# Kernel tuning notes

Hardware: AMD Instinct MI355X
Metric: run time of the kernel (lower is better)

Reference implementation:

```python
import jax, jax.numpy as jnp
import numpy as np

N_NODES = 50000
N_EDGES = 800000
EMB = 128
N_LAYERS = 2
BN_EPS = 1e-5


def setup_inputs() -> dict:
    key = jax.random.key(0)
    ks = jax.random.split(key, 16)
    N, E, D, L = N_NODES, N_EDGES, EMB, N_LAYERS
    x = jax.random.randint(ks[0], (N, 2), 0, 3)
    edge_index = jax.random.randint(ks[1], (2, E), 0, N)
    edge_attr = jax.random.randint(ks[2], (E, 2), 0, 3)
    batch = jnp.zeros((N,), dtype=jnp.int32)
    s = 0.1
    xemb1 = jax.random.normal(ks[3], (120, D)) * s   # atom-type embedding
    xemb2 = jax.random.normal(ks[4], (3, D)) * s     # chirality embedding
    e1 = jax.random.normal(ks[5], (L, 7, D)) * s     # bond-type embedding per layer
    e2 = jax.random.normal(ks[6], (L, 3, D)) * s     # bond-direction embedding per layer
    W1 = jax.random.normal(ks[7], (L, D, 2 * D)) * s
    b1 = jnp.zeros((L, 2 * D))
    W2 = jax.random.normal(ks[8], (L, 2 * D, D)) * s
    b2 = jnp.zeros((L, D))
    gamma = jnp.ones((L, D))
    beta = jnp.zeros((L, D))
    return {"x": x, "edge_index": edge_index, "edge_attr": edge_attr, "batch": batch,
            "xemb1": xemb1, "xemb2": xemb2, "e1": e1, "e2": e2,
            "W1": W1, "b1": b1, "W2": W2, "b2": b2, "gamma": gamma, "beta": beta}


def _gnn_forward(x, edge_index, edge_attr, xemb1, xemb2, e1, e2, W1, b1, W2, b2, gamma, beta):
    N = x.shape[0]
    # add self loops; self-loop edge_attr = [4, 0]
    loop = jnp.arange(N, dtype=edge_index.dtype)
    src = jnp.concatenate([edge_index[0], loop])
    dst = jnp.concatenate([edge_index[1], loop])
    loop_attr = jnp.concatenate([jnp.full((N, 1), 4, dtype=edge_attr.dtype),
                                 jnp.zeros((N, 1), dtype=edge_attr.dtype)], axis=1)
    ea = jnp.concatenate([edge_attr, loop_attr], axis=0)  # [E+N, 2]

    # input node embedding
    h = xemb1[x[:, 0]] + xemb2[x[:, 1]]  # [N, D]

    for l in range(N_LAYERS):
        eemb = e1[l][ea[:, 0]] + e2[l][ea[:, 1]]      # [E+N, D]
        msg = h[src] + eemb                            # gather + edge fuse
        agg = jax.ops.segment_sum(msg, dst, num_segments=N)  # scatter-add
        # GIN update MLP: Linear -> ReLU -> Linear
        h2 = jax.nn.relu(agg @ W1[l] + b1[l]) @ W2[l] + b2[l]
        # BatchNorm1d (training mode: biased batch stats)
        mu = jnp.mean(h2, axis=0)
        var = jnp.mean(jnp.square(h2 - mu), axis=0)
        h2 = gamma[l] * (h2 - mu) * jax.lax.rsqrt(var + BN_EPS) + beta[l]
        # dropout(relu) for non-final layers; drop_ratio=0 -> identity dropout
        h = h2 if l == N_LAYERS - 1 else jax.nn.relu(h2)
    return h  # JK='last'


def reference(x, edge_index, edge_attr, batch, xemb1, xemb2, e1, e2, W1, b1, W2, b2, gamma, beta):
    return _gnn_forward(x, edge_index, edge_attr, xemb1, xemb2, e1, e2, W1, b1, W2, b2, gamma, beta)
```

## Files before the change

### kernel.cpp

```cpp
#include <hip/hip_runtime.h>
#include <stdint.h>

#define N_NODES 50000
#define N_EDGES 800000
#define EMB 128
#define NPAD 50176
#define MBLK 392
#define BN_EPS 1e-5f
#define SENT_KEY ((N_NODES << 5) | 21)
#define NODES_PER_XCD 6250
#define XCHUNK 2048
#define NCHUNKS ((N_EDGES + XCHUNK - 1) / XCHUNK)

typedef __attribute__((ext_vector_type(8))) short short8;
typedef __attribute__((ext_vector_type(4))) float f32x4;

__device__ __forceinline__ float bf2f(unsigned short u) {
    return __uint_as_float(((unsigned int)u) << 16);
}
__device__ __forceinline__ unsigned short f2bf(float f) {
    unsigned int u = __float_as_uint(f);
    u += 0x7fffu + ((u >> 16) & 1u);
    return (unsigned short)(u >> 16);
}
__device__ __forceinline__ float bflo(unsigned int v) { return __uint_as_float(v << 16); }
__device__ __forceinline__ float bfhi(unsigned int v) { return __uint_as_float(v & 0xffff0000u); }
__device__ __forceinline__ unsigned int packbf(float lo, float hi) {
    return (unsigned int)f2bf(lo) | ((unsigned int)f2bf(hi) << 16);
}

__global__ void k_prep(const int* __restrict__ x, const float* __restrict__ xe1,
                       const float* __restrict__ xe2, unsigned int* __restrict__ h,
                       const float* __restrict__ W1, const float* __restrict__ W2,
                       unsigned short* __restrict__ w1t, unsigned short* __restrict__ w2t,
                       int* __restrict__ deg,
                       const int* __restrict__ ei, const int* __restrict__ ea,
                       int* __restrict__ keyv, float* __restrict__ bnsum) {
    int idx = blockIdx.x * 256 + threadIdx.x;
    int i = idx >> 6, j = idx & 63;
    if (i < N_NODES) {
        int a = x[2 * i], c = x[2 * i + 1];
        float2 va = *(const float2*)(xe1 + a * EMB + j * 2);
        float2 vb = *(const float2*)(xe2 + c * EMB + j * 2);
        h[i * 64 + j] = packbf(va.x + vb.x, va.y + vb.y);
    } else if (i == N_NODES) {
        h[(size_t)i * 64 + j] = 0u;
    }
    if (idx < 4 * 32768) {
        int sec = idx >> 15, q = idx & 32767;
        if (sec < 2) {
            int r = q >> 8, c = q & 255;
            w1t[sec * 32768 + c * 128 + r] = f2bf(W1[sec * 32768 + q]);
        } else {
            int s = sec - 2;
            int r = q >> 7, c = q & 127;
            w2t[s * 32768 + c * 256 + r] = f2bf(W2[s * 32768 + q]);
        }
    }
    if (idx < N_EDGES) {
        int2 aa = *(const int2*)(ea + 2 * idx);
        keyv[idx] = (ei[idx] << 5) | (aa.x * 3 + aa.y);
    }
    if (idx < N_NODES) deg[idx] = 0;
    if (idx < 256) bnsum[idx] = 0.f;
}

__global__ void k_hist(const int* __restrict__ dst, int* __restrict__ deg) {
    int xcd = blockIdx.x & 7, chunk = blockIdx.x >> 3;
    int lo = xcd * NODES_PER_XCD, hi = lo + NODES_PER_XCD;
    int e0 = chunk * XCHUNK + threadIdx.x * 4;
#pragma unroll
    for (int it = 0; it < XCHUNK / 1024; ++it) {
        int e = e0 + it * 1024;
        if (e < N_EDGES) {
            int4 d4 = *(const int4*)(dst + e);
            if (d4.x >= lo && d4.x < hi) atomicAdd(&deg[d4.x], 1);
            if (d4.y >= lo && d4.y < hi) atomicAdd(&deg[d4.y], 1);
            if (d4.z >= lo && d4.z < hi) atomicAdd(&deg[d4.z], 1);
            if (d4.w >= lo && d4.w < hi) atomicAdd(&deg[d4.w], 1);
        }
    }
}

__global__ void k_scan1(const int* __restrict__ deg, int* __restrict__ part, int* __restrict__ bsums) {
    __shared__ int wsum[16];
    int lane = threadIdx.x & 63, wid = threadIdx.x >> 6;
    int i = blockIdx.x * 1024 + threadIdx.x;
    int d = (i < N_NODES) ? deg[i] : 0;
    int v = (d + 15) & ~15;
    int s = v;
#pragma unroll
    for (int off = 1; off < 64; off <<= 1) {
        int t = __shfl_up(s, off);
        if (lane >= off) s += t;
    }
    if (lane == 63) wsum[wid] = s;
    __syncthreads();
    if (wid == 0) {
        int w = (lane < 16) ? wsum[lane] : 0;
#pragma unroll
        for (int off = 1; off < 16; off <<= 1) {
            int t = __shfl_up(w, off);
            if (lane >= off) w += t;
        }
        if (lane < 16) wsum[lane] = w;
    }
    __syncthreads();
    int base = (wid > 0) ? wsum[wid - 1] : 0;
    if (i < N_NODES) part[i] = base + s - v;
    if (threadIdx.x == 1023) bsums[blockIdx.x] = wsum[15];
}

__global__ void k_scan3(const int* __restrict__ part, const int* __restrict__ bsums,
                        const int* __restrict__ deg, int* __restrict__ offs,
                        int* __restrict__ cursor, int* __restrict__ keys) {
    __shared__ int bs[64];
    int tid = threadIdx.x;
    if (tid < 64) {
        int v = (tid < 49) ? bsums[tid] : 0;
        int orig = v;
#pragma unroll
        for (int off = 1; off < 64; off <<= 1) {
            int t = __shfl_up(v, off);
            if (tid >= off) v += t;
        }
        bs[tid] = v - orig;
    }
    __syncthreads();
    int i = blockIdx.x * 256 + tid;
    if (i >= N_NODES) return;
    int o = part[i] + bs[i >> 10];
    offs[i] = o;
    cursor[i] = o;
    int d = deg[i], pd = (d + 15) & ~15;
    for (int j = d; j < pd; ++j) keys[o + j] = SENT_KEY;
    if (i == N_NODES - 1) offs[N_NODES] = o + pd;
}

__global__ void k_fill(const int* __restrict__ dst, const int* __restrict__ keyv,
                       int* __restrict__ cursor, int* __restrict__ keys) {
    int xcd = blockIdx.x & 7, chunk = blockIdx.x >> 3;
    int lo = xcd * NODES_PER_XCD, hi = lo + NODES_PER_XCD;
    int e0 = chunk * XCHUNK + threadIdx.x * 4;
#pragma unroll
    for (int it = 0; it < XCHUNK / 1024; ++it) {
        int e = e0 + it * 1024;
        if (e < N_EDGES) {
            int4 d4 = *(const int4*)(dst + e);
            int dv[4] = {d4.x, d4.y, d4.z, d4.w};
#pragma unroll
            for (int q = 0; q < 4; ++q) {
                int d = dv[q];
                if (d >= lo && d < hi) {
                    int p = atomicAdd(&cursor[d], 1);
                    keys[p] = keyv[e + q];
                }
            }
        }
    }
}

__global__ __launch_bounds__(256) void k_agg(
    const unsigned int* __restrict__ h,
    const int* __restrict__ offs,
    const int* __restrict__ keys,
    const float* __restrict__ e1l, const float* __restrict__ e2l,
    unsigned int* __restrict__ agg)
{
    __shared__ float e12[22 * 132];
    for (int t = threadIdx.x; t < 22 * 128; t += 256) {
        int combo = t >> 7, f = t & 127;
        float v = 0.f;
        if (combo < 21) {
            int a0 = combo / 3, a1 = combo - a0 * 3;
            v = e1l[a0 * EMB + f] + e2l[a1 * EMB + f];
        }
        e12[combo * 132 + f] = v;
    }
    __syncthreads();
    int wave = threadIdx.x >> 6, lane = threadIdx.x & 63;
    int sub = lane >> 4, fl = lane & 15;
    int node = blockIdx.x * 16 + wave * 4 + sub;
    float ax[8] = {0.f, 0.f, 0.f, 0.f, 0.f, 0.f, 0.f, 0.f};
    int o = 0, nch = 0;
    if (node < N_NODES) {
        o = offs[node];
        nch = (offs[node + 1] - o) >> 4;
        uint4 hv = *(const uint4*)(h + (size_t)node * 64 + fl * 4);
        const float* ep = e12 + 12 * 132 + fl * 8;
        float4 e0 = *(const float4*)ep, e1_ = *(const float4*)(ep + 4);
        ax[0] = bflo(hv.x) + e0.x;  ax[1] = bfhi(hv.x) + e0.y;
        ax[2] = bflo(hv.y) + e0.z;  ax[3] = bfhi(hv.y) + e0.w;
        ax[4] = bflo(hv.z) + e1_.x; ax[5] = bfhi(hv.z) + e1_.y;
        ax[6] = bflo(hv.w) + e1_.z; ax[7] = bfhi(hv.w) + e1_.w;
    }
    int maxch = nch;
#pragma unroll
    for (int d = 32; d; d >>= 1) maxch = max(maxch, __shfl_xor(maxch, d));
    int key = (0 < nch) ? keys[o + fl] : SENT_KEY;
    for (int c = 0; c < maxch; ++c) {
        int keyn = (c + 1 < nch) ? keys[o + (c + 1) * 16 + fl] : SENT_KEY;
#pragma unroll
        for (int j = 0; j < 16; ++j) {
            int kj = __shfl(key, sub * 16 + j);
            uint4 g = *(const uint4*)(h + (size_t)(kj >> 5) * 64 + fl * 4);
            const float* ep = e12 + (kj & 31) * 132 + fl * 8;
            float4 e0 = *(const float4*)ep, e1_ = *(const float4*)(ep + 4);
            ax[0] += bflo(g.x) + e0.x;  ax[1] += bfhi(g.x) + e0.y;
            ax[2] += bflo(g.y) + e0.z;  ax[3] += bfhi(g.y) + e0.w;
            ax[4] += bflo(g.z) + e1_.x; ax[5] += bfhi(g.z) + e1_.y;
            ax[6] += bflo(g.w) + e1_.z; ax[7] += bfhi(g.w) + e1_.w;
        }
        key = keyn;
    }
    if (node < NPAD) {
        uint4 out;
        out.x = packbf(ax[0], ax[1]); out.y = packbf(ax[2], ax[3]);
        out.z = packbf(ax[4], ax[5]); out.w = packbf(ax[6], ax[7]);
        *(uint4*)(agg + (size_t)node * 64 + fl * 4) = out;
    }
}

__global__ __launch_bounds__(256, 2) void k_mlp(
    unsigned short* aggh2,
    const unsigned short* __restrict__ w1t,
    const float* __restrict__ b1,
    const unsigned short* __restrict__ w2t,
    const float* __restrict__ b2,
    float* __restrict__ bnsum)
{
    __shared__ float bn[256];
    int lane = threadIdx.x & 63;
    int wave = threadIdx.x >> 6;
    int quad = lane >> 4, r16 = lane & 15;
    int m0 = (blockIdx.x * 4 + wave) * 32;
    int sel  = (lane >> 5) & 1;
    int srcA = ((lane >> 4) & 1) * 32 + r16;
    int srcB = srcA + 16;
    bn[threadIdx.x] = 0.f;

    short8 bagg[2][4];
#pragma unroll
    for (int t = 0; t < 2; ++t)
#pragma unroll
        for (int c = 0; c < 4; ++c)
            bagg[t][c] = *(const short8*)(aggh2 + (size_t)(m0 + t * 16 + r16) * 128 + c * 32 + quad * 8);

    float b2v[8];
#pragma unroll
    for (int n = 0; n < 8; ++n) b2v[n] = b2[n * 16 + r16];

    f32x4 acc2[2][8];
#pragma unroll
    for (int t = 0; t < 2; ++t)
#pragma unroll
        for (int n = 0; n < 8; ++n) acc2[t][n] = (f32x4){0.f, 0.f, 0.f, 0.f};

    for (int c2 = 0; c2 < 8; ++c2) {
        unsigned int pk[2][2][2];
#pragma unroll
        for (int ntl = 0; ntl < 2; ++ntl) {
            int nt = c2 * 2 + ntl;
            short8 aw[4];
#pragma unroll
            for (int c = 0; c < 4; ++c)
                aw[c] = *(const short8*)(w1t + (nt * 16 + r16) * 128 + c * 32 + quad * 8);
            float4 bv = *(const float4*)(b1 + nt * 16 + quad * 4);
#pragma unroll
            for (int t = 0; t < 2; ++t) {
                f32x4 a1 = {0.f, 0.f, 0.f, 0.f};
#pragma unroll
                for (int c = 0; c < 4; ++c)
                    a1 = __builtin_amdgcn_mfma_f32_16x16x32_bf16(aw[c], bagg[t][c], a1, 0, 0, 0);
                float v0 = a1[0] + bv.x; v0 = v0 > 0.f ? v0 : 0.f;
                float v1 = a1[1] + bv.y; v1 = v1 > 0.f ? v1 : 0.f;
                float v2 = a1[2] + bv.z; v2 = v2 > 0.f ? v2 : 0.f;
                float v3 = a1[3] + bv.w; v3 = v3 > 0.f ? v3 : 0.f;
                pk[ntl][t][0] = packbf(v0, v1);
                pk[ntl][t][1] = packbf(v2, v3);
            }
        }
        short8 a2f[2];
#pragma unroll
        for (int t = 0; t < 2; ++t) {
            int u0 = __shfl((int)pk[0][t][0], srcA), w0 = __shfl((int)pk[1][t][0], srcA);
            int u1 = __shfl((int)pk[0][t][1], srcA), w1_ = __shfl((int)pk[1][t][1], srcA);
            int u2 = __shfl((int)pk[0][t][0], srcB), w2_ = __shfl((int)pk[1][t][0], srcB);
            int u3 = __shfl((int)pk[0][t][1], srcB), w3_ = __shfl((int)pk[1][t][1], srcB);
            union { int i[4]; short8 s; } a2u;
            a2u.i[0] = sel ? w0 : u0;
            a2u.i[1] = sel ? w1_ : u1;
            a2u.i[2] = sel ? w2_ : u2;
            a2u.i[3] = sel ? w3_ : u3;
            a2f[t] = a2u.s;
        }
#pragma unroll
        for (int n = 0; n < 8; ++n) {
            short8 bw = *(const short8*)(w2t + (n * 16 + r16) * 256 + c2 * 32 + quad * 8);
            acc2[0][n] = __builtin_amdgcn_mfma_f32_16x16x32_bf16(a2f[0], bw, acc2[0][n], 0, 0, 0);
            acc2[1][n] = __builtin_amdgcn_mfma_f32_16x16x32_bf16(a2f[1], bw, acc2[1][n], 0, 0, 0);
        }
    }
    float s[8], q[8];
#pragma unroll
    for (int n = 0; n < 8; ++n) { s[n] = 0.f; q[n] = 0.f; }
#pragma unroll
    for (int t = 0; t < 2; ++t)
#pragma unroll
        for (int n = 0; n < 8; ++n)
#pragma unroll
            for (int r = 0; r < 4; ++r) {
                int row = m0 + t * 16 + quad * 4 + r;
                float v = acc2[t][n][r] + b2v[n];
                if (row < N_NODES) {
                    aggh2[(size_t)row * 128 + n * 16 + r16] = f2bf(v);
                    s[n] += v; q[n] += v * v;
                }
            }
#pragma unroll
    for (int n = 0; n < 8; ++n) {
        s[n] += __shfl_xor(s[n], 16); q[n] += __shfl_xor(q[n], 16);
        s[n] += __shfl_xor(s[n], 32); q[n] += __shfl_xor(q[n], 32);
    }
    __syncthreads();
    if (quad == 0) {
#pragma unroll
        for (int n = 0; n < 8; ++n) {
            atomicAdd(&bn[n * 16 + r16], s[n]);
            atomicAdd(&bn[128 + n * 16 + r16], q[n]);
        }
    }
    __syncthreads();
    atomicAdd(&bnsum[threadIdx.x], bn[threadIdx.x]);
}

__global__ void k_bnred(float* __restrict__ bnsum, const float* __restrict__ gamma,
                        const float* __restrict__ beta, float* __restrict__ ab) {
    int tid = threadIdx.x;
    float s = 0.f, q = 0.f;
    if (tid < 128) { s = bnsum[tid]; q = bnsum[128 + tid]; }
    __syncthreads();
    bnsum[tid] = 0.f;
    if (tid < 128) {
        float mean = s * (1.f / N_NODES);
        float var  = q * (1.f / N_NODES) - mean * mean;
        float rstd = rsqrtf(var + BN_EPS);
        float g = gamma[tid];
        ab[tid]       = g * rstd;
        ab[128 + tid] = beta[tid] - mean * g * rstd;
    }
}

__global__ void k_bnnorm(const unsigned int* __restrict__ h2, const float* __restrict__ ab,
                         unsigned int* __restrict__ outb, float2* __restrict__ outf, int mode) {
    int idx = blockIdx.x * 256 + threadIdx.x;
    if (idx >= N_NODES * 64) return;
    int p = idx & 63;
    int c0 = 2 * p, c1 = 2 * p + 1;
    float a0 = ab[c0], a1 = ab[c1], s0 = ab[128 + c0], s1 = ab[128 + c1];
    unsigned int hv = h2[idx];
    float a = bflo(hv) * a0 + s0;
    float b = bfhi(hv) * a1 + s1;
    if (mode == 0) {
        a = a > 0.f ? a : 0.f;
        b = b > 0.f ? b : 0.f;
        outb[idx] = packbf(a, b);
    } else {
        outf[idx] = make_float2(a, b);
    }
}

extern "C" void kernel_launch(void* const* d_in, const int* in_sizes, int n_in,
                              void* d_out, int out_size, void* d_ws, size_t ws_size,
                              hipStream_t stream) {
    const int* x  = (const int*)d_in[0];
    const int* ei = (const int*)d_in[1];
    const int* ea = (const int*)d_in[2];
    const float* xe1 = (const float*)d_in[4];
    const float* xe2 = (const float*)d_in[5];
    const float* e1  = (const float*)d_in[6];
    const float* e2  = (const float*)d_in[7];
    const float* W1  = (const float*)d_in[8];
    const float* b1  = (const float*)d_in[9];
    const float* W2  = (const float*)d_in[10];
    const float* b2  = (const float*)d_in[11];
    const float* gm  = (const float*)d_in[12];
    const float* bt  = (const float*)d_in[13];

    char* ws = (char*)d_ws;
    size_t off = 0;
    auto take = [&](size_t bytes) -> char* {
        char* p = ws + off;
        off = (off + bytes + 255) & ~(size_t)255;
        return p;
    };
    unsigned int* h_buf = (unsigned int*)take((size_t)(N_NODES + 1) * 64 * 4);
    unsigned int* aggb  = (unsigned int*)take((size_t)NPAD * 64 * 4);
    unsigned short* w1t = (unsigned short*)take((size_t)2 * 32768 * 2);
    unsigned short* w2t = (unsigned short*)take((size_t)2 * 32768 * 2);
    int* deg    = (int*)take((size_t)N_NODES * 4);
    int* offs   = (int*)take((size_t)(N_NODES + 1) * 4);
    int* cursor = (int*)take((size_t)N_NODES * 4);
    int* keys   = (int*)take((size_t)(N_EDGES + N_NODES * 16) * 4);
    int* keyv   = (int*)take((size_t)N_EDGES * 4);
    int* bsums  = (int*)take(64 * 4);
    float* bnsum = (float*)take(256 * 4);
    float* ab   = (float*)take(256 * 4);

    k_prep<<<((N_NODES + 1) * 64 + 255) / 256, 256, 0, stream>>>(x, xe1, xe2, h_buf,
                                                                 W1, W2, w1t, w2t, deg,
                                                                 ei, ea, keyv, bnsum);
    k_hist<<<8 * NCHUNKS, 256, 0, stream>>>(ei + N_EDGES, deg);
    k_scan1<<<49, 1024, 0, stream>>>(deg, offs, bsums);
    k_scan3<<<(N_NODES + 255) / 256, 256, 0, stream>>>(offs, bsums, deg, offs, cursor, keys);
    k_fill<<<8 * NCHUNKS, 256, 0, stream>>>(ei + N_EDGES, keyv, cursor, keys);

    for (int l = 0; l < 2; ++l) {
        k_agg<<<NPAD / 16, 256, 0, stream>>>(h_buf, offs, keys,
                                             e1 + l * 896, e2 + l * 384, aggb);
        k_mlp<<<MBLK, 256, 0, stream>>>((unsigned short*)aggb, w1t + l * 32768, b1 + l * 256,
                                        w2t + l * 32768, b2 + l * 128, bnsum);
        k_bnred<<<1, 256, 0, stream>>>(bnsum, gm + l * 128, bt + l * 128, ab);
        k_bnnorm<<<(N_NODES * 64) / 256, 256, 0, stream>>>(aggb, ab, h_buf, (float2*)d_out, l);
    }
}
```

Baseline: 378.7 us.

## Sort nodes by degree bucket for aggregation and fuse BN reduce into normalize

Nodes are bucketed by their padded chunk count, and a permutation is built so that each wave in the aggregation kernel processes nodes of similar degree, which reduces divergence from the max-chunk loop. The separate single-block BN reduction kernel is folded into the normalize kernel, which recomputes scale and shift per block and processes eight features per thread with vectorized loads and stores. Per-layer BN sum buffers remove the need to re-zero between layers. In exchange the aggregation kernel adds an indirect node lookup, and its output ordering must still match row indices.

```diff
diff --git a/kernel.cpp b/kernel.cpp
--- a/kernel.cpp
+++ b/kernel.cpp
@@ -11,13 +11,11 @@
 #define NODES_PER_XCD 6250
 #define XCHUNK 2048
 #define NCHUNKS ((N_EDGES + XCHUNK - 1) / XCHUNK)
+#define PBLK 196
 
 typedef __attribute__((ext_vector_type(8))) short short8;
 typedef __attribute__((ext_vector_type(4))) float f32x4;
 
-__device__ __forceinline__ float bf2f(unsigned short u) {
-    return __uint_as_float(((unsigned int)u) << 16);
-}
 __device__ __forceinline__ unsigned short f2bf(float f) {
     unsigned int u = __float_as_uint(f);
     u += 0x7fffu + ((u >> 16) & 1u);
@@ -35,7 +33,8 @@
                        unsigned short* __restrict__ w1t, unsigned short* __restrict__ w2t,
                        int* __restrict__ deg,
                        const int* __restrict__ ei, const int* __restrict__ ea,
-                       int* __restrict__ keyv, float* __restrict__ bnsum) {
+                       int* __restrict__ keyv, float* __restrict__ bnsum,
+                       int* __restrict__ bmeta) {
     int idx = blockIdx.x * 256 + threadIdx.x;
     int i = idx >> 6, j = idx & 63;
     if (i < N_NODES) {
@@ -62,7 +61,8 @@
         keyv[idx] = (ei[idx] << 5) | (aa.x * 3 + aa.y);
     }
     if (idx < N_NODES) deg[idx] = 0;
-    if (idx < 256) bnsum[idx] = 0.f;
+    if (idx < 512) bnsum[idx] = 0.f;
+    if (idx < 16) bmeta[idx] = 0;
 }
 
 __global__ void k_hist(const int* __restrict__ dst, int* __restrict__ deg) {
@@ -113,9 +113,12 @@
 
 __global__ void k_scan3(const int* __restrict__ part, const int* __restrict__ bsums,
                         const int* __restrict__ deg, int* __restrict__ offs,
-                        int* __restrict__ cursor, int* __restrict__ keys) {
+                        int* __restrict__ cursor, int* __restrict__ keys,
+                        int* __restrict__ bcnt) {
     __shared__ int bs[64];
+    __shared__ int lc[8];
     int tid = threadIdx.x;
+    if (tid < 8) lc[tid] = 0;
     if (tid < 64) {
         int v = (tid < 49) ? bsums[tid] : 0;
         int orig = v;
@@ -128,17 +131,24 @@
     }
     __syncthreads();
     int i = blockIdx.x * 256 + tid;
-    if (i >= N_NODES) return;
-    int o = part[i] + bs[i >> 10];
-    offs[i] = o;
-    cursor[i] = o;
-    int d = deg[i], pd = (d + 15) & ~15;
-    for (int j = d; j < pd; ++j) keys[o + j] = SENT_KEY;
-    if (i == N_NODES - 1) offs[N_NODES] = o + pd;
+    if (i < N_NODES) {
+        int o = part[i] + bs[i >> 10];
+        offs[i] = o;
+        cursor[i] = o;
+        int d = deg[i], pd = (d + 15) & ~15;
+        for (int j = d; j < pd; ++j) keys[o + j] = SENT_KEY;
+        if (i == N_NODES - 1) offs[N_NODES] = o + pd;
+        int nch = pd >> 4;
+        atomicAdd(&lc[nch > 7 ? 7 : nch], 1);
+    }
+    __syncthreads();
+    if (tid < 8) atomicAdd(&bcnt[tid], lc[tid]);
 }
 
 __global__ void k_fill(const int* __restrict__ dst, const int* __restrict__ keyv,
-                       int* __restrict__ cursor, int* __restrict__ keys) {
+                       int* __restrict__ cursor, int* __restrict__ keys,
+                       const int* __restrict__ deg, const int* __restrict__ bcnt,
+                       int* __restrict__ bcur, int* __restrict__ perm) {
     int xcd = blockIdx.x & 7, chunk = blockIdx.x >> 3;
     int lo = xcd * NODES_PER_XCD, hi = lo + NODES_PER_XCD;
     int e0 = chunk * XCHUNK + threadIdx.x * 4;
@@ -158,12 +168,34 @@
             }
         }
     }
+    if (blockIdx.x < PBLK) {
+        __shared__ int lcnt[8], gbase[8], tbase[8];
+        if (threadIdx.x < 8) lcnt[threadIdx.x] = 0;
+        __syncthreads();
+        int i = blockIdx.x * 256 + threadIdx.x;
+        int b = 0, lrank = 0;
+        if (i < N_NODES) {
+            int nch = (deg[i] + 15) >> 4;
+            b = nch > 7 ? 7 : nch;
+            lrank = atomicAdd(&lcnt[b], 1);
+        }
+        __syncthreads();
+        if (threadIdx.x < 8) {
+            gbase[threadIdx.x] = atomicAdd(&bcur[threadIdx.x], lcnt[threadIdx.x]);
+            int s = 0;
+            for (int k = 0; k < threadIdx.x; ++k) s += bcnt[k];
+            tbase[threadIdx.x] = s;
+        }
+        __syncthreads();
+        if (i < N_NODES) perm[tbase[b] + gbase[b] + lrank] = i;
+    }
 }
 
 __global__ __launch_bounds__(256) void k_agg(
     const unsigned int* __restrict__ h,
     const int* __restrict__ offs,
     const int* __restrict__ keys,
+    const int* __restrict__ perm,
     const float* __restrict__ e1l, const float* __restrict__ e2l,
     unsigned int* __restrict__ agg)
 {
@@ -180,7 +212,8 @@
     __syncthreads();
     int wave = threadIdx.x >> 6, lane = threadIdx.x & 63;
     int sub = lane >> 4, fl = lane & 15;
-    int node = blockIdx.x * 16 + wave * 4 + sub;
+    int slot = blockIdx.x * 16 + wave * 4 + sub;
+    int node = (slot < N_NODES) ? perm[slot] : slot;
     float ax[8] = {0.f, 0.f, 0.f, 0.f, 0.f, 0.f, 0.f, 0.f};
     int o = 0, nch = 0;
     if (node < N_NODES) {
@@ -213,7 +246,7 @@
         }
         key = keyn;
     }
-    if (node < NPAD) {
+    {
         uint4 out;
         out.x = packbf(ax[0], ax[1]); out.y = packbf(ax[2], ax[3]);
         out.z = packbf(ax[4], ax[5]); out.w = packbf(ax[6], ax[7]);
@@ -334,39 +367,44 @@
     atomicAdd(&bnsum[threadIdx.x], bn[threadIdx.x]);
 }
 
-__global__ void k_bnred(float* __restrict__ bnsum, const float* __restrict__ gamma,
-                        const float* __restrict__ beta, float* __restrict__ ab) {
+__global__ void k_bnnorm(const uint4* __restrict__ h2, const float* __restrict__ bnsum,
+                         const float* __restrict__ gamma, const float* __restrict__ beta,
+                         uint4* __restrict__ outb, float4* __restrict__ outf, int mode) {
+    __shared__ float ab[256];
     int tid = threadIdx.x;
-    float s = 0.f, q = 0.f;
-    if (tid < 128) { s = bnsum[tid]; q = bnsum[128 + tid]; }
-    __syncthreads();
-    bnsum[tid] = 0.f;
     if (tid < 128) {
-        float mean = s * (1.f / N_NODES);
-        float var  = q * (1.f / N_NODES) - mean * mean;
+        float mean = bnsum[tid] * (1.f / N_NODES);
+        float var  = bnsum[128 + tid] * (1.f / N_NODES) - mean * mean;
         float rstd = rsqrtf(var + BN_EPS);
         float g = gamma[tid];
         ab[tid]       = g * rstd;
         ab[128 + tid] = beta[tid] - mean * g * rstd;
     }
-}
-
-__global__ void k_bnnorm(const unsigned int* __restrict__ h2, const float* __restrict__ ab,
-                         unsigned int* __restrict__ outb, float2* __restrict__ outf, int mode) {
-    int idx = blockIdx.x * 256 + threadIdx.x;
-    if (idx >= N_NODES * 64) return;
-    int p = idx & 63;
-    int c0 = 2 * p, c1 = 2 * p + 1;
-    float a0 = ab[c0], a1 = ab[c1], s0 = ab[128 + c0], s1 = ab[128 + c1];
-    unsigned int hv = h2[idx];
-    float a = bflo(hv) * a0 + s0;
-    float b = bfhi(hv) * a1 + s1;
+    __syncthreads();
+    int idx = blockIdx.x * 256 + tid;
+    if (idx >= N_NODES * 16) return;
+    int p = (idx & 15) * 8;
+    uint4 hv = h2[idx];
+    float v0 = bflo(hv.x) * ab[p + 0] + ab[128 + p + 0];
+    float v1 = bfhi(hv.x) * ab[p + 1] + ab[128 + p + 1];
+    float v2 = bflo(hv.y) * ab[p + 2] + ab[128 + p + 2];
+    float v3 = bfhi(hv.y) * ab[p + 3] + ab[128 + p + 3];
+    float v4 = bflo(hv.z) * ab[p + 4] + ab[128 + p + 4];
+    float v5 = bfhi(hv.z) * ab[p + 5] + ab[128 + p + 5];
+    float v6 = bflo(hv.w) * ab[p + 6] + ab[128 + p + 6];
+    float v7 = bfhi(hv.w) * ab[p + 7] + ab[128 + p + 7];
     if (mode == 0) {
-        a = a > 0.f ? a : 0.f;
-        b = b > 0.f ? b : 0.f;
-        outb[idx] = packbf(a, b);
+        v0 = v0 > 0.f ? v0 : 0.f; v1 = v1 > 0.f ? v1 : 0.f;
+        v2 = v2 > 0.f ? v2 : 0.f; v3 = v3 > 0.f ? v3 : 0.f;
+        v4 = v4 > 0.f ? v4 : 0.f; v5 = v5 > 0.f ? v5 : 0.f;
+        v6 = v6 > 0.f ? v6 : 0.f; v7 = v7 > 0.f ? v7 : 0.f;
+        uint4 out;
+        out.x = packbf(v0, v1); out.y = packbf(v2, v3);
+        out.z = packbf(v4, v5); out.w = packbf(v6, v7);
+        outb[idx] = out;
     } else {
-        outf[idx] = make_float2(a, b);
+        outf[2 * idx]     = make_float4(v0, v1, v2, v3);
+        outf[2 * idx + 1] = make_float4(v4, v5, v6, v7);
     }
 }
 
@@ -404,23 +442,27 @@
     int* keys   = (int*)take((size_t)(N_EDGES + N_NODES * 16) * 4);
     int* keyv   = (int*)take((size_t)N_EDGES * 4);
     int* bsums  = (int*)take(64 * 4);
-    float* bnsum = (float*)take(256 * 4);
-    float* ab   = (float*)take(256 * 4);
+    float* bnsum = (float*)take(512 * 4);
+    int* bmeta  = (int*)take(16 * 4);
+    int* perm   = (int*)take((size_t)N_NODES * 4);
+    int* bcnt = bmeta, *bcur = bmeta + 8;
 
     k_prep<<<((N_NODES + 1) * 64 + 255) / 256, 256, 0, stream>>>(x, xe1, xe2, h_buf,
                                                                  W1, W2, w1t, w2t, deg,
-                                                                 ei, ea, keyv, bnsum);
+                                                                 ei, ea, keyv, bnsum, bmeta);
     k_hist<<<8 * NCHUNKS, 256, 0, stream>>>(ei + N_EDGES, deg);
     k_scan1<<<49, 1024, 0, stream>>>(deg, offs, bsums);
-    k_scan3<<<(N_NODES + 255) / 256, 256, 0, stream>>>(offs, bsums, deg, offs, cursor, keys);
-    k_fill<<<8 * NCHUNKS, 256, 0, stream>>>(ei + N_EDGES, keyv, cursor, keys);
+    k_scan3<<<(N_NODES + 255) / 256, 256, 0, stream>>>(offs, bsums, deg, offs, cursor, keys, bcnt);
+    k_fill<<<8 * NCHUNKS, 256, 0, stream>>>(ei + N_EDGES, keyv, cursor, keys,
+                                            deg, bcnt, bcur, perm);
 
     for (int l = 0; l < 2; ++l) {
-        k_agg<<<NPAD / 16, 256, 0, stream>>>(h_buf, offs, keys,
+        k_agg<<<NPAD / 16, 256, 0, stream>>>(h_buf, offs, keys, perm,
                                              e1 + l * 896, e2 + l * 384, aggb);
         k_mlp<<<MBLK, 256, 0, stream>>>((unsigned short*)aggb, w1t + l * 32768, b1 + l * 256,
-                                        w2t + l * 32768, b2 + l * 128, bnsum);
-        k_bnred<<<1, 256, 0, stream>>>(bnsum, gm + l * 128, bt + l * 128, ab);
-        k_bnnorm<<<(N_NODES * 64) / 256, 256, 0, stream>>>(aggb, ab, h_buf, (float2*)d_out, l);
-    }
-}
+                                        w2t + l * 32768, b2 + l * 128, bnsum + l * 256);
+        k_bnnorm<<<(N_NODES * 16 + 255) / 256, 256, 0, stream>>>((const uint4*)aggb, bnsum + l * 256,
+                                                                 gm + l * 128, bt + l * 128,
+                                                                 (uint4*)h_buf, (float4*)d_out, l);
+    }
+}
```

New measurement: 382.9 us. Within noise of the previous version (+1.1%).
